# Kernel tuning notes

Hardware: AMD Instinct MI355X
Metric: run time of the kernel (lower is better)

The kernel has to match this reference:

```python
import jax, jax.numpy as jnp
import numpy as np

N_NODES = 100000


def sage_conv(x, src, dst, W_l, W_r, b, num_nodes):
    """PyG SAGEConv (aggr='mean', root_weight=True): x@W_l + mean_j(x_j)@W_r + b."""
    msgs = x[src]  # [E, d] irregular gather
    summed = jax.ops.segment_sum(msgs, dst, num_segments=num_nodes)  # [N, d]
    cnt = jax.ops.segment_sum(jnp.ones((src.shape[0],), x.dtype), dst,
                              num_segments=num_nodes)  # [N]
    mean = summed / jnp.maximum(cnt, 1.0)[:, None]
    return x @ W_l + mean @ W_r + b


def setup_inputs() -> dict:
    key = jax.random.key(0)
    ks = jax.random.split(key, 6)
    x = jax.random.normal(ks[0], (N_NODES, 256), dtype=jnp.float32)
    edge_index = jax.random.randint(ks[1], (2, 1600000), 0, N_NODES, dtype=jnp.int32)
    W1_l = jax.random.normal(ks[2], (256, 64), dtype=jnp.float32) * (1.0 / np.sqrt(256))
    W1_r = jax.random.normal(ks[3], (256, 64), dtype=jnp.float32) * (1.0 / np.sqrt(256))
    b1 = jnp.zeros((64,), jnp.float32)
    W2_l = jax.random.normal(ks[4], (64, 40), dtype=jnp.float32) * (1.0 / np.sqrt(64))
    W2_r = jax.random.normal(ks[5], (64, 40), dtype=jnp.float32) * (1.0 / np.sqrt(64))
    b2 = jnp.zeros((40,), jnp.float32)
    return {"x": x, "edge_index": edge_index, "W1_l": W1_l, "W1_r": W1_r,
            "b1": b1, "W2_l": W2_l, "W2_r": W2_r, "b2": b2}


def reference(x, edge_index, W1_l, W1_r, b1, W2_l, W2_r, b2):
    src, dst = edge_index[0], edge_index[1]
    n = x.shape[0]
    h = sage_conv(x, src, dst, W1_l, W1_r, b1, n)
    h = jax.nn.relu(h)
    # F.dropout(training=self.training) -> identity at inference
    h = sage_conv(h, src, dst, W2_l, W2_r, b2, n)
    return jax.nn.softmax(h, axis=1)
```

## Files before the change

### kernel.cpp

```cpp
#include <hip/hip_runtime.h>
#include <hip/hip_bf16.h>
#include <math.h>


typedef __attribute__((ext_vector_type(8))) short bf16x8;
typedef __attribute__((ext_vector_type(4))) float f32x4;

static __device__ __forceinline__ unsigned short f2bf(float f) {
    unsigned int u = __builtin_bit_cast(unsigned int, f);
    unsigned int r = (u + 0x7FFFu + ((u >> 16) & 1u)) >> 16;
    return (unsigned short)r;
}
static __device__ __forceinline__ float bf2f(unsigned short u) {
    unsigned int v = ((unsigned int)u) << 16;
    return __builtin_bit_cast(float, v);
}


__global__ void k_count(const int* __restrict__ dst, int* __restrict__ cnt, int E) {
    int e = blockIdx.x * blockDim.x + threadIdx.x;
    if (e < E) atomicAdd(&cnt[dst[e]], 1);
}

__global__ void k_blocksum(const int* __restrict__ cnt, int* __restrict__ bsum, int N) {
    __shared__ int sm[256];
    int i = blockIdx.x * 256 + threadIdx.x;
    sm[threadIdx.x] = (i < N) ? cnt[i] : 0;
    __syncthreads();
    for (int s = 128; s > 0; s >>= 1) {
        if (threadIdx.x < s) sm[threadIdx.x] += sm[threadIdx.x + s];
        __syncthreads();
    }
    if (threadIdx.x == 0) bsum[blockIdx.x] = sm[0];
}

__global__ void k_scanbsum(int* __restrict__ bsum, int nb) {
    __shared__ int a[512], b[512];
    int t = threadIdx.x;
    int v = (t < nb) ? bsum[t] : 0;
    a[t] = v;
    __syncthreads();
    int* pin = a; int* pout = b;
    for (int o = 1; o < 512; o <<= 1) {
        pout[t] = (t >= o) ? pin[t] + pin[t - o] : pin[t];
        __syncthreads();
        int* tmp = pin; pin = pout; pout = tmp;
    }
    if (t < nb) bsum[t] = pin[t] - v;
}

__global__ void k_scanfinal(const int* __restrict__ cnt, const int* __restrict__ bsum,
                            int* __restrict__ off, int* __restrict__ cursor, int N) {
    __shared__ int a[256], b[256];
    int t = threadIdx.x;
    int i = blockIdx.x * 256 + t;
    int v = (i < N) ? cnt[i] : 0;
    a[t] = v;
    __syncthreads();
    int* pin = a; int* pout = b;
    for (int o = 1; o < 256; o <<= 1) {
        pout[t] = (t >= o) ? pin[t] + pin[t - o] : pin[t];
        __syncthreads();
        int* tmp = pin; pin = pout; pout = tmp;
    }
    if (i < N) {
        int ex = bsum[blockIdx.x] + pin[t] - v;
        off[i] = ex;
        cursor[i] = ex;
    }
}

__global__ void k_scatterp(const int* __restrict__ src, const int* __restrict__ dst,
                           int* __restrict__ cursor, int* __restrict__ csr,
                           int E, int range) {
    int e = blockIdx.x * blockDim.x + threadIdx.x;
    if (e < E) {
        int d = dst[e];
        int lo = blockIdx.y * range;
        if (d >= lo && d < lo + range) {
            int pos = atomicAdd(&cursor[d], 1);
            csr[pos] = src[e];
        }
    }
}


__global__ __launch_bounds__(256) void k_gemm1(const float* __restrict__ x,
                                               const float* __restrict__ Wl,
                                               const float* __restrict__ Wr,
                                               float* __restrict__ y1l,
                                               unsigned short* __restrict__ y1r, int N) {
    __shared__ unsigned short xs[64][40];
    __shared__ unsigned short wsm[128][40];
    int tid = threadIdx.x;
    int row0 = blockIdx.x * 64;
    int lane = tid & 63;
    int wid = tid >> 6;
    int wm = wid >> 1;
    int wn = wid & 1;

    int xr = tid >> 2;
    int xq = tid & 3;
    int wc = tid >> 1;
    int wo = tid & 1;
    const float* wsrc = (wc < 64) ? (Wl + wc) : (Wr + (wc - 64));

    f32x4 acc[2][4];
    #pragma unroll
    for (int m = 0; m < 2; ++m)
        #pragma unroll
        for (int n = 0; n < 4; ++n) acc[m][n] = (f32x4){0.f, 0.f, 0.f, 0.f};

    for (int kk = 0; kk < 256; kk += 32) {
        {
            int grow = row0 + xr;
            float4 v0 = make_float4(0.f, 0.f, 0.f, 0.f);
            float4 v1 = make_float4(0.f, 0.f, 0.f, 0.f);
            if (grow < N) {
                const float* p = x + (size_t)grow * 256 + kk + xq * 8;
                v0 = *(const float4*)(p);
                v1 = *(const float4*)(p + 4);
            }
            bf16x8 pk;
            pk[0] = (short)f2bf(v0.x); pk[1] = (short)f2bf(v0.y);
            pk[2] = (short)f2bf(v0.z); pk[3] = (short)f2bf(v0.w);
            pk[4] = (short)f2bf(v1.x); pk[5] = (short)f2bf(v1.y);
            pk[6] = (short)f2bf(v1.z); pk[7] = (short)f2bf(v1.w);
            *(bf16x8*)(&xs[xr][xq * 8]) = pk;
        }
        {
            bf16x8 w0, w1;
            #pragma unroll
            for (int j = 0; j < 8; ++j)
                w0[j] = (short)f2bf(wsrc[(size_t)(kk + wo * 16 + j) * 64]);
            #pragma unroll
            for (int j = 0; j < 8; ++j)
                w1[j] = (short)f2bf(wsrc[(size_t)(kk + wo * 16 + 8 + j) * 64]);
            *(bf16x8*)(&wsm[wc][wo * 16])     = w0;
            *(bf16x8*)(&wsm[wc][wo * 16 + 8]) = w1;
        }
        __syncthreads();

        int fr = lane & 15;
        int ko = (lane >> 4) * 8;
        bf16x8 a0 = *(const bf16x8*)(&xs[wm * 32 + fr][ko]);
        bf16x8 a1 = *(const bf16x8*)(&xs[wm * 32 + 16 + fr][ko]);
        bf16x8 b0 = *(const bf16x8*)(&wsm[wn * 64 + fr][ko]);
        bf16x8 b1 = *(const bf16x8*)(&wsm[wn * 64 + 16 + fr][ko]);
        bf16x8 b2 = *(const bf16x8*)(&wsm[wn * 64 + 32 + fr][ko]);
        bf16x8 b3 = *(const bf16x8*)(&wsm[wn * 64 + 48 + fr][ko]);

        acc[0][0] = __builtin_amdgcn_mfma_f32_16x16x32_bf16(a0, b0, acc[0][0], 0, 0, 0);
        acc[0][1] = __builtin_amdgcn_mfma_f32_16x16x32_bf16(a0, b1, acc[0][1], 0, 0, 0);
        acc[0][2] = __builtin_amdgcn_mfma_f32_16x16x32_bf16(a0, b2, acc[0][2], 0, 0, 0);
        acc[0][3] = __builtin_amdgcn_mfma_f32_16x16x32_bf16(a0, b3, acc[0][3], 0, 0, 0);
        acc[1][0] = __builtin_amdgcn_mfma_f32_16x16x32_bf16(a1, b0, acc[1][0], 0, 0, 0);
        acc[1][1] = __builtin_amdgcn_mfma_f32_16x16x32_bf16(a1, b1, acc[1][1], 0, 0, 0);
        acc[1][2] = __builtin_amdgcn_mfma_f32_16x16x32_bf16(a1, b2, acc[1][2], 0, 0, 0);
        acc[1][3] = __builtin_amdgcn_mfma_f32_16x16x32_bf16(a1, b3, acc[1][3], 0, 0, 0);
        __syncthreads();
    }

    int cn = lane & 15;
    int r4 = (lane >> 4) * 4;
    #pragma unroll
    for (int m = 0; m < 2; ++m) {
        #pragma unroll
        for (int r = 0; r < 4; ++r) {
            int row = row0 + wm * 32 + m * 16 + r4 + r;
            if (row < N) {
                if (wn == 0) {
                    float* yp = y1l + (size_t)row * 64 + cn;
                    yp[0]  = acc[m][0][r];
                    yp[16] = acc[m][1][r];
                    yp[32] = acc[m][2][r];
                    yp[48] = acc[m][3][r];
                } else {
                    unsigned short* yq = y1r + (size_t)row * 64 + cn;
                    yq[0]  = f2bf(acc[m][0][r]);
                    yq[16] = f2bf(acc[m][1][r]);
                    yq[32] = f2bf(acc[m][2][r]);
                    yq[48] = f2bf(acc[m][3][r]);
                }
            }
        }
    }
}


__global__ __launch_bounds__(256) void k_fused2(const float* __restrict__ y1l,
                                                const unsigned short* __restrict__ y1r,
                                                const int* __restrict__ csr,
                                                const int* __restrict__ off,
                                                const int* __restrict__ cnt,
                                                const float* __restrict__ b1,
                                                const float* __restrict__ W2l,
                                                const float* __restrict__ W2r,
                                                float* __restrict__ y2l,
                                                unsigned short* __restrict__ y2r, int N) {
    __shared__ float wsm[64][80];
    __shared__ float hrow[4][64];
    int tid = threadIdx.x;
    #pragma unroll
    for (int it = 0; it < 5; ++it) {
        int idx = tid + it * 256;
        int k = idx / 20;
        int cq = idx % 20;
        const float* s = (cq < 10) ? (W2l + (size_t)k * 40 + cq * 4)
                                   : (W2r + (size_t)k * 40 + (cq - 10) * 4);
        *(float4*)(&wsm[k][cq * 4]) = *(const float4*)s;
    }
    __syncthreads();

    int lane = tid & 63;
    int wv = tid >> 6;
    int wid = blockIdx.x * 4 + wv;
    int nw = gridDim.x * 4;
    float bl = b1[lane];
    int cl = (lane < 40) ? 2 * lane : 0;

    for (int i = wid; i < N; i += nw) {
        int deg = cnt[i];
        int start = off[i];
        float a0 = 0.f, a1 = 0.f, a2 = 0.f, a3 = 0.f;
        for (int base = 0; base < deg; base += 64) {
            int m = min(64, deg - base);
            int s = (lane < m) ? csr[start + base + lane] : 0;
            int j = 0;
            for (; j + 4 <= m; j += 4) {
                int s0 = __shfl(s, j), s1 = __shfl(s, j + 1);
                int s2 = __shfl(s, j + 2), s3 = __shfl(s, j + 3);
                a0 += bf2f(y1r[(size_t)s0 * 64 + lane]);
                a1 += bf2f(y1r[(size_t)s1 * 64 + lane]);
                a2 += bf2f(y1r[(size_t)s2 * 64 + lane]);
                a3 += bf2f(y1r[(size_t)s3 * 64 + lane]);
            }
            for (; j < m; ++j) {
                int sj = __shfl(s, j);
                a0 += bf2f(y1r[(size_t)sj * 64 + lane]);
            }
        }
        float mean = (a0 + a1 + a2 + a3) / (float)max(deg, 1);
        float hv = fmaxf(y1l[(size_t)i * 64 + lane] + mean + bl, 0.f);

        hrow[wv][lane] = hv;
        float p0 = 0.f, p1 = 0.f;
        #pragma unroll
        for (int k4 = 0; k4 < 64; k4 += 4) {
            float4 hk = *(const float4*)(&hrow[wv][k4]);
            float2 w0 = *(const float2*)(&wsm[k4 + 0][cl]);
            float2 w1 = *(const float2*)(&wsm[k4 + 1][cl]);
            float2 w2 = *(const float2*)(&wsm[k4 + 2][cl]);
            float2 w3 = *(const float2*)(&wsm[k4 + 3][cl]);
            p0 += hk.x * w0.x + hk.y * w1.x + hk.z * w2.x + hk.w * w3.x;
            p1 += hk.x * w0.y + hk.y * w1.y + hk.z * w2.y + hk.w * w3.y;
        }
        if (lane < 20) {
            *(float2*)(y2l + (size_t)i * 40 + cl) = make_float2(p0, p1);
        } else if (lane < 40) {
            unsigned int pk = (unsigned int)f2bf(p0) | ((unsigned int)f2bf(p1) << 16);
            *(unsigned int*)(y2r + (size_t)i * 40 + (cl - 40)) = pk;
        }
    }
}


__global__ void k_agg2(const float* __restrict__ y2l,
                       const unsigned short* __restrict__ y2r,
                       const int* __restrict__ csr,
                       const int* __restrict__ off, const int* __restrict__ cnt,
                       const float* __restrict__ b2, float* __restrict__ out, int N) {
    int lane = threadIdx.x & 63;
    int wid = (blockIdx.x * blockDim.x + threadIdx.x) >> 6;
    int nw = (gridDim.x * blockDim.x) >> 6;
    for (int i = wid; i < N; i += nw) {
        int deg = cnt[i];
        int start = off[i];
        float a0 = 0.f, a1 = 0.f, a2 = 0.f, a3 = 0.f;
        bool act = (lane < 40);
        for (int base = 0; base < deg; base += 64) {
            int m = min(64, deg - base);
            int s = (lane < m) ? csr[start + base + lane] : 0;
            int j = 0;
            for (; j + 4 <= m; j += 4) {
                int s0 = __shfl(s, j), s1 = __shfl(s, j + 1);
                int s2 = __shfl(s, j + 2), s3 = __shfl(s, j + 3);
                if (act) {
                    a0 += bf2f(y2r[(size_t)s0 * 40 + lane]);
                    a1 += bf2f(y2r[(size_t)s1 * 40 + lane]);
                    a2 += bf2f(y2r[(size_t)s2 * 40 + lane]);
                    a3 += bf2f(y2r[(size_t)s3 * 40 + lane]);
                }
            }
            for (; j < m; ++j) {
                int sj = __shfl(s, j);
                if (act) a0 += bf2f(y2r[(size_t)sj * 40 + lane]);
            }
        }
        float logit = -INFINITY;
        if (act) {
            float mean = (a0 + a1 + a2 + a3) / (float)max(deg, 1);
            logit = y2l[(size_t)i * 40 + lane] + mean + b2[lane];
        }
        float mx = logit;
        #pragma unroll
        for (int o = 32; o > 0; o >>= 1) mx = fmaxf(mx, __shfl_xor(mx, o));
        float e = act ? expf(logit - mx) : 0.f;
        float se = e;
        #pragma unroll
        for (int o = 32; o > 0; o >>= 1) se += __shfl_xor(se, o);
        if (act) out[(size_t)i * 40 + lane] = e / se;
    }
}


extern "C" void kernel_launch(void* const* d_in, const int* in_sizes, int n_in,
                              void* d_out, int out_size, void* d_ws, size_t ws_size,
                              hipStream_t stream) {
    const float* x   = (const float*)d_in[0];
    const int*   ei  = (const int*)d_in[1];
    const float* W1l = (const float*)d_in[2];
    const float* W1r = (const float*)d_in[3];
    const float* b1  = (const float*)d_in[4];
    const float* W2l = (const float*)d_in[5];
    const float* W2r = (const float*)d_in[6];
    const float* b2  = (const float*)d_in[7];
    float* out = (float*)d_out;

    int N = in_sizes[0] / 256;
    int E = in_sizes[1] / 2;
    const int* srcp = ei;
    const int* dstp = ei + E;

    char* w = (char*)d_ws;
    auto alloc = [&](size_t bytes) {
        char* p = w;
        w += (bytes + 255) & ~(size_t)255;
        return p;
    };
    int nb = (N + 255) / 256;
    int*            cnt    = (int*)alloc((size_t)N * 4);
    int*            off    = (int*)alloc((size_t)N * 4);
    int*            cursor = (int*)alloc((size_t)N * 4);
    int*            bsum   = (int*)alloc((size_t)nb * 4);
    int*            csr    = (int*)alloc((size_t)E * 4);
    float*          y1l    = (float*)alloc((size_t)N * 64 * 4);
    unsigned short* y1r    = (unsigned short*)alloc((size_t)N * 64 * 2);
    float*          y2l    = (float*)alloc((size_t)N * 40 * 4);
    unsigned short* y2r    = (unsigned short*)alloc((size_t)N * 40 * 2);

    hipMemsetAsync(cnt, 0, (size_t)N * 4, stream);
    k_count<<<(E + 255) / 256, 256, 0, stream>>>(dstp, cnt, E);
    k_blocksum<<<nb, 256, 0, stream>>>(cnt, bsum, N);
    k_scanbsum<<<1, 512, 0, stream>>>(bsum, nb);
    k_scanfinal<<<nb, 256, 0, stream>>>(cnt, bsum, off, cursor, N);

    const int P = 4;
    int range = (N + P - 1) / P;
    dim3 sgrid((E + 255) / 256, P);
    k_scatterp<<<sgrid, 256, 0, stream>>>(srcp, dstp, cursor, csr, E, range);

    k_gemm1<<<(N + 63) / 64, 256, 0, stream>>>(x, W1l, W1r, y1l, y1r, N);
    k_fused2<<<1792, 256, 0, stream>>>(y1l, y1r, csr, off, cnt, b1, W2l, W2r, y2l, y2r, N);
    k_agg2<<<2048, 256, 0, stream>>>(y2l, y2r, csr, off, cnt, b2, out, N);
}
```

Before: 450.4 us.

## Gather packed bf16 pairs in layer-1 aggregation and store layer-2 outputs interleaved fp32

```diff
diff --git a/kernel.cpp b/kernel.cpp
--- a/kernel.cpp
+++ b/kernel.cpp
@@ -11,8 +11,8 @@
     unsigned int r = (u + 0x7FFFu + ((u >> 16) & 1u)) >> 16;
     return (unsigned short)r;
 }
-static __device__ __forceinline__ float bf2f(unsigned short u) {
-    unsigned int v = ((unsigned int)u) << 16;
+static __device__ __forceinline__ float bf2f(unsigned int lo16) {
+    unsigned int v = lo16 << 16;
     return __builtin_bit_cast(float, v);
 }
 
@@ -189,15 +189,14 @@
 
 
 __global__ __launch_bounds__(256) void k_fused2(const float* __restrict__ y1l,
-                                                const unsigned short* __restrict__ y1r,
+                                                const unsigned int* __restrict__ y1ru,
                                                 const int* __restrict__ csr,
                                                 const int* __restrict__ off,
                                                 const int* __restrict__ cnt,
                                                 const float* __restrict__ b1,
                                                 const float* __restrict__ W2l,
                                                 const float* __restrict__ W2r,
-                                                float* __restrict__ y2l,
-                                                unsigned short* __restrict__ y2r, int N) {
+                                                float* __restrict__ y2, int N) {
     __shared__ float wsm[64][80];
     __shared__ float hrow[4][64];
     int tid = threadIdx.x;
@@ -213,6 +212,8 @@
     __syncthreads();
 
     int lane = tid & 63;
+    int half = lane >> 5;
+    int fl = lane & 31;
     int wv = tid >> 6;
     int wid = blockIdx.x * 4 + wv;
     int nw = gridDim.x * 4;
@@ -222,29 +223,39 @@
     for (int i = wid; i < N; i += nw) {
         int deg = cnt[i];
         int start = off[i];
-        float a0 = 0.f, a1 = 0.f, a2 = 0.f, a3 = 0.f;
+        float p0 = 0.f, p1 = 0.f;
         for (int base = 0; base < deg; base += 64) {
             int m = min(64, deg - base);
             int s = (lane < m) ? csr[start + base + lane] : 0;
-            int j = 0;
-            for (; j + 4 <= m; j += 4) {
-                int s0 = __shfl(s, j), s1 = __shfl(s, j + 1);
-                int s2 = __shfl(s, j + 2), s3 = __shfl(s, j + 3);
-                a0 += bf2f(y1r[(size_t)s0 * 64 + lane]);
-                a1 += bf2f(y1r[(size_t)s1 * 64 + lane]);
-                a2 += bf2f(y1r[(size_t)s2 * 64 + lane]);
-                a3 += bf2f(y1r[(size_t)s3 * 64 + lane]);
-            }
-            for (; j < m; ++j) {
-                int sj = __shfl(s, j);
-                a0 += bf2f(y1r[(size_t)sj * 64 + lane]);
-            }
-        }
-        float mean = (a0 + a1 + a2 + a3) / (float)max(deg, 1);
+            int pairs = (m + 1) >> 1;
+            int t = 0;
+            for (; t + 2 <= pairs; t += 2) {
+                int e0 = 2 * t + half;
+                int e1 = e0 + 2;
+                int s0 = __shfl(s, e0);
+                int s1 = __shfl(s, e1);
+                unsigned int u0 = y1ru[(size_t)s0 * 32 + fl];
+                unsigned int u1 = y1ru[(size_t)s1 * 32 + fl];
+                if (e0 < m) { p0 += bf2f(u0 & 0xffffu); p1 += bf2f(u0 >> 16); }
+                if (e1 < m) { p0 += bf2f(u1 & 0xffffu); p1 += bf2f(u1 >> 16); }
+            }
+            for (; t < pairs; ++t) {
+                int e0 = 2 * t + half;
+                int s0 = __shfl(s, e0);
+                unsigned int u0 = y1ru[(size_t)s0 * 32 + fl];
+                if (e0 < m) { p0 += bf2f(u0 & 0xffffu); p1 += bf2f(u0 >> 16); }
+            }
+        }
+        p0 += __shfl_xor(p0, 32);
+        p1 += __shfl_xor(p1, 32);
+        float q0 = __shfl(p0, lane >> 1);
+        float q1 = __shfl(p1, lane >> 1);
+        float sum = (lane & 1) ? q1 : q0;
+        float mean = sum / (float)max(deg, 1);
         float hv = fmaxf(y1l[(size_t)i * 64 + lane] + mean + bl, 0.f);
 
         hrow[wv][lane] = hv;
-        float p0 = 0.f, p1 = 0.f;
+        float g0 = 0.f, g1 = 0.f;
         #pragma unroll
         for (int k4 = 0; k4 < 64; k4 += 4) {
             float4 hk = *(const float4*)(&hrow[wv][k4]);
@@ -252,22 +263,16 @@
             float2 w1 = *(const float2*)(&wsm[k4 + 1][cl]);
             float2 w2 = *(const float2*)(&wsm[k4 + 2][cl]);
             float2 w3 = *(const float2*)(&wsm[k4 + 3][cl]);
-            p0 += hk.x * w0.x + hk.y * w1.x + hk.z * w2.x + hk.w * w3.x;
-            p1 += hk.x * w0.y + hk.y * w1.y + hk.z * w2.y + hk.w * w3.y;
-        }
-        if (lane < 20) {
-            *(float2*)(y2l + (size_t)i * 40 + cl) = make_float2(p0, p1);
-        } else if (lane < 40) {
-            unsigned int pk = (unsigned int)f2bf(p0) | ((unsigned int)f2bf(p1) << 16);
-            *(unsigned int*)(y2r + (size_t)i * 40 + (cl - 40)) = pk;
-        }
-    }
-}
-
-
-__global__ void k_agg2(const float* __restrict__ y2l,
-                       const unsigned short* __restrict__ y2r,
-                       const int* __restrict__ csr,
+            g0 += hk.x * w0.x + hk.y * w1.x + hk.z * w2.x + hk.w * w3.x;
+            g1 += hk.x * w0.y + hk.y * w1.y + hk.z * w2.y + hk.w * w3.y;
+        }
+        if (lane < 40)
+            *(float2*)(y2 + (size_t)i * 80 + cl) = make_float2(g0, g1);
+    }
+}
+
+
+__global__ void k_agg2(const float* __restrict__ y2, const int* __restrict__ csr,
                        const int* __restrict__ off, const int* __restrict__ cnt,
                        const float* __restrict__ b2, float* __restrict__ out, int N) {
     int lane = threadIdx.x & 63;
@@ -286,21 +291,21 @@
                 int s0 = __shfl(s, j), s1 = __shfl(s, j + 1);
                 int s2 = __shfl(s, j + 2), s3 = __shfl(s, j + 3);
                 if (act) {
-                    a0 += bf2f(y2r[(size_t)s0 * 40 + lane]);
-                    a1 += bf2f(y2r[(size_t)s1 * 40 + lane]);
-                    a2 += bf2f(y2r[(size_t)s2 * 40 + lane]);
-                    a3 += bf2f(y2r[(size_t)s3 * 40 + lane]);
+                    a0 += y2[(size_t)s0 * 80 + 40 + lane];
+                    a1 += y2[(size_t)s1 * 80 + 40 + lane];
+                    a2 += y2[(size_t)s2 * 80 + 40 + lane];
+                    a3 += y2[(size_t)s3 * 80 + 40 + lane];
                 }
             }
             for (; j < m; ++j) {
                 int sj = __shfl(s, j);
-                if (act) a0 += bf2f(y2r[(size_t)sj * 40 + lane]);
+                if (act) a0 += y2[(size_t)sj * 80 + 40 + lane];
             }
         }
         float logit = -INFINITY;
         if (act) {
             float mean = (a0 + a1 + a2 + a3) / (float)max(deg, 1);
-            logit = y2l[(size_t)i * 40 + lane] + mean + b2[lane];
+            logit = y2[(size_t)i * 80 + lane] + mean + b2[lane];
         }
         float mx = logit;
         #pragma unroll
@@ -346,8 +351,7 @@
     int*            csr    = (int*)alloc((size_t)E * 4);
     float*          y1l    = (float*)alloc((size_t)N * 64 * 4);
     unsigned short* y1r    = (unsigned short*)alloc((size_t)N * 64 * 2);
-    float*          y2l    = (float*)alloc((size_t)N * 40 * 4);
-    unsigned short* y2r    = (unsigned short*)alloc((size_t)N * 40 * 2);
+    float*          y2     = (float*)alloc((size_t)N * 80 * 4);
 
     hipMemsetAsync(cnt, 0, (size_t)N * 4, stream);
     k_count<<<(E + 255) / 256, 256, 0, stream>>>(dstp, cnt, E);
@@ -361,6 +365,7 @@
     k_scatterp<<<sgrid, 256, 0, stream>>>(srcp, dstp, cursor, csr, E, range);
 
     k_gemm1<<<(N + 63) / 64, 256, 0, stream>>>(x, W1l, W1r, y1l, y1r, N);
-    k_fused2<<<1792, 256, 0, stream>>>(y1l, y1r, csr, off, cnt, b1, W2l, W2r, y2l, y2r, N);
-    k_agg2<<<2048, 256, 0, stream>>>(y2l, y2r, csr, off, cnt, b2, out, N);
-}
+    k_fused2<<<1792, 256, 0, stream>>>(y1l, (const unsigned int*)y1r, csr, off, cnt,
+                                       b1, W2l, W2r, y2, N);
+    k_agg2<<<2048, 256, 0, stream>>>(y2, csr, off, cnt, b2, out, N);
+}
```

Result: faster. 386.7 us (-14.1%).
